# Kernel tuning notes

Hardware: AMD Instinct MI355X
Metric: run time of the kernel (lower is better)

The kernel has to match this reference:

```python
import jax, jax.numpy as jnp
import numpy as np

V, D, DC, L, K, H, ND, S, B = 16, 256, 128, 3, 16, 4, 3, 900, 16
HD = D // H
DMETA = 17           # [confidence(1) | layer_id(8) | iter(4) | pass(4)]
DSLOT = DC + DMETA
MAX_ITERS, MAX_PASSES, WRITE_TOK = 2, 2, 64
FLOATS = ['token_embed','segment_embed','slot_embeddings','layer_id_embeddings',
          'Wq_read','Wk_read','Wv_read','Wg_read','bg_read','Wqkv','Wo',
          'Wwk','Wwv','Wwg','bwg','Wout','bout','prev_answer_embed','Wfb','bfb']


def setup_inputs():
    key = jax.random.key(0)
    ks = jax.random.split(key, 24)
    n = lambda i, shape: 0.02 * jax.random.normal(ks[i], shape, dtype=jnp.float32)
    return dict(
        demo_inputs=jax.random.randint(ks[0], (B, ND, S), 0, V),
        demo_outputs=jax.random.randint(ks[1], (B, ND, S), 0, V),
        test_input=jax.random.randint(ks[2], (B, S), 0, V),
        token_embed=n(3, (V, D)), segment_embed=n(4, (2, D)),
        slot_embeddings=n(5, (L, K, DC)), layer_id_embeddings=n(6, (L, 8)),
        Wq_read=n(7, (L, D, DC)), Wk_read=n(8, (L, DSLOT, DC)), Wv_read=n(9, (L, DSLOT, D)),
        Wg_read=n(10, (L, D, 1)), bg_read=jnp.zeros((L, 1)),
        Wqkv=n(11, (L, D, 3 * D)), Wo=n(12, (L, D, D)),
        Wwk=n(13, (L, D, DC)), Wwv=n(14, (L, D, DC)),
        Wwg=n(15, (L, 2 * DC, 1)), bwg=jnp.zeros((L, 1)),
        Wout=n(16, (D, V)), bout=jnp.zeros((V,)),
        prev_answer_embed=n(17, (V, D)),
        Wfb=n(18, (2 * D, D)), bfb=jnp.zeros((D,)),
    )


def make_rope(n, hd):
    inv = 1.0 / (10000.0 ** (jnp.arange(0, hd, 2, dtype=jnp.float32) / hd))
    f = jnp.arange(n, dtype=jnp.float32)[:, None] * inv[None, :]  # [N, hd/2]
    return jnp.cos(f), jnp.sin(f)


def apply_rope(x, cos, sin):  # x: [B,H,N,hd]
    x1, x2 = x[..., ::2], x[..., 1::2]
    r1 = x1 * cos - x2 * sin
    r2 = x1 * sin + x2 * cos
    return jnp.stack([r1, r2], axis=-1).reshape(x.shape)


def layer_step(h, cache, l, it, pas, cos, sin, p):
    Bsz, N, _ = h.shape
    s0 = l * K
    # --- read: cross-attention from sequence to full structured cache ---
    q = h @ p['Wq_read'][l]                                   # [B,N,DC]
    k = cache @ p['Wk_read'][l]                               # [B,LK,DC]
    v = cache @ p['Wv_read'][l]                               # [B,LK,D]
    attn = jax.nn.softmax(jnp.einsum('bnd,bmd->bnm', q, k) / np.float32(np.sqrt(DC)), axis=-1)
    read = jnp.einsum('bnm,bmd->bnd', attn, v)
    rgate = jax.nn.sigmoid(h @ p['Wg_read'][l] + p['bg_read'][l])
    h = h + rgate * read
    # --- linear self-attention with RoPE (use_linear_attention=True) ---
    qh, kh, vh = jnp.split(h @ p['Wqkv'][l], 3, axis=-1)
    heads = lambda x: x.reshape(Bsz, N, H, HD).transpose(0, 2, 1, 3)
    qh, kh, vh = heads(qh), heads(kh), heads(vh)
    qf = jax.nn.elu(apply_rope(qh, cos, sin)) + 1.0
    kf = jax.nn.elu(apply_rope(kh, cos, sin)) + 1.0
    kv = jnp.einsum('bhnd,bhne->bhde', kf, vh)                # [B,H,HD,HD]
    z = 1.0 / (jnp.einsum('bhnd,bhd->bhn', qf, kf.sum(axis=2)) + 1e-6)
    att = jnp.einsum('bhnd,bhde->bhne', qf, kv) * z[..., None]
    h = h + att.transpose(0, 2, 1, 3).reshape(Bsz, N, D) @ p['Wo'][l]
    # --- write: last max_write_tokens tokens -> this layer's slot block ---
    wt = h[:, -WRITE_TOK:]                                    # [B,64,D]
    wk, wv = wt @ p['Wwk'][l], wt @ p['Wwv'][l]               # [B,64,DC]
    sq = cache[:, s0:s0 + K, :DC]                             # slot content queries
    wattn = jax.nn.softmax(jnp.einsum('bkd,bmd->bkm', sq, wk) / np.float32(np.sqrt(DC)), axis=-1)
    new_c = jnp.einsum('bkm,bmd->bkd', wattn, wv)
    wgate = jax.nn.sigmoid(jnp.concatenate([sq, new_c], -1) @ p['Wwg'][l] + p['bwg'][l])
    it_oh = jax.nn.one_hot(min(it, 3), 4, dtype=h.dtype)
    ps_oh = jax.nn.one_hot(min(pas, 3), 4, dtype=h.dtype)
    cache = cache.at[:, s0:s0 + K, :DC].set(sq + wgate * new_c)
    cache = cache.at[:, s0:s0 + K, DC:DC + 1].set(wgate)      # confidence
    cache = cache.at[:, s0:s0 + K, DC + 9:DC + 13].set(jnp.broadcast_to(it_oh, (Bsz, K, 4)))
    cache = cache.at[:, s0:s0 + K, DC + 13:].set(jnp.broadcast_to(ps_oh, (Bsz, K, 4)))
    return h, cache


def _model(p, demo_inputs, demo_outputs, test_input):
    Bsz = test_input.shape[0]
    # interleave demo_in/demo_out pairs then append test input
    demos = jnp.stack([demo_inputs, demo_outputs], axis=2).reshape(Bsz, ND * 2 * S)
    full = jnp.concatenate([demos, test_input], axis=1)       # [B, 6300]
    N = full.shape[1]
    cur = p['token_embed'][full] + p['segment_embed'][0]      # [B,N,D]
    cos, sin = make_rope(N, HD)
    # initial cache: learned content | conf=0 | layer_id | iter=0 | pass=0
    content = jnp.broadcast_to(p['slot_embeddings'].reshape(L * K, DC), (Bsz, L * K, DC))
    lids = jnp.broadcast_to(p['layer_id_embeddings'][:, None, :], (L, K, 8)).reshape(L * K, 8)
    meta = jnp.concatenate([jnp.zeros((L * K, 1)), lids, jnp.zeros((L * K, 8))], axis=-1)
    cache = jnp.concatenate([content, jnp.broadcast_to(meta, (Bsz, L * K, DMETA))], axis=-1)
    ts = ND * 2 * S
    prev_logits = None
    for pas in range(MAX_PASSES):
        if pas > 0:  # answer feedback from previous pass predictions
            pae = p['prev_answer_embed'][jnp.argmax(prev_logits, axis=-1)]
            tr = cur[:, ts:ts + S]
            g = jax.nn.sigmoid(jnp.concatenate([tr, pae], -1) @ p['Wfb'] + p['bfb'])
            cur = cur.at[:, ts:ts + S].set(tr + g * pae)
        h = cur
        for l in range(L):
            for it in range(MAX_ITERS):
                h, cache = layer_step(h, cache, l, it, pas, cos, sin, p)
        prev_logits = h[:, ts:ts + S] @ p['Wout'] + p['bout']  # [B,S,V]
    return prev_logits


def reference(demo_inputs, demo_outputs, test_input, token_embed, segment_embed,
              slot_embeddings, layer_id_embeddings, Wq_read, Wk_read, Wv_read,
              Wg_read, bg_read, Wqkv, Wo, Wwk, Wwv, Wwg, bwg, Wout, bout,
              prev_answer_embed, Wfb, bfb):
    p = dict(zip(FLOATS, (token_embed, segment_embed, slot_embeddings, layer_id_embeddings,
                          Wq_read, Wk_read, Wv_read, Wg_read, bg_read, Wqkv, Wo,
                          Wwk, Wwv, Wwg, bwg, Wout, bout, prev_answer_embed, Wfb, bfb)))
    return _model(p, demo_inputs, demo_outputs, test_input)
```

## Files before the change

kernel.cpp:

```cpp
#include <hip/hip_runtime.h>
#include <math.h>

#define Bz 16
#define Sz 900
#define Vz 16
#define Dz 256
#define DCz 128
#define Hz 4
#define Nz 6300
#define TSz 5400
#define DSLOTz 145
#define NSLOTz 48
#define GXA 99

typedef unsigned short u16;
typedef unsigned int u32;

typedef __bf16 bf16x8 __attribute__((ext_vector_type(8)));
typedef float floatx4 __attribute__((ext_vector_type(4)));
union U8 { bf16x8 v; uint4 q; };

static __device__ __forceinline__ float sigm(float x){ return 1.0f/(1.0f+__expf(-x)); }
static __device__ __forceinline__ void fma4(float4& a, float s, float4 b){ a.x+=s*b.x; a.y+=s*b.y; a.z+=s*b.z; a.w+=s*b.w; }
static __device__ __forceinline__ float dot4(float4 a, float4 b){ return a.x*b.x + a.y*b.y + a.z*b.z + a.w*b.w; }
static __device__ __forceinline__ float4 f4z(){ float4 z; z.x=0.f; z.y=0.f; z.z=0.f; z.w=0.f; return z; }
static __device__ __forceinline__ float elu1(float x){ return x>0.f ? x+1.f : __expf(x); }
static __device__ __forceinline__ float fcomp(float4 v, int i){ return (i==0)?v.x:(i==1)?v.y:(i==2)?v.z:v.w; }

static __device__ __forceinline__ uint hi16(float x){
  uint u = __float_as_uint(x);
  return (u + 0x7fffu + ((u>>16)&1u)) >> 16;
}

typedef const void GV __attribute__((address_space(1)));
typedef void LV __attribute__((address_space(3)));
static __device__ __forceinline__ void gl16(const float* g, float* l){
  __builtin_amdgcn_global_load_lds((GV*)g, (LV*)l, 16, 0, 0);
}
static __device__ __forceinline__ void gl16b(const void* g, void* l){
  __builtin_amdgcn_global_load_lds((GV*)g, (LV*)l, 16, 0, 0);
}

__global__ void k_sentinel(float* out, int nelem){
  int i = blockIdx.x*256 + threadIdx.x;
  if (i < nelem) out[i] = 12345.0f;
}

__global__ void k_zero(float* p, int n){
  int i = blockIdx.x*256 + threadIdx.x;
  if (i < n) p[i] = 0.f;
}

__global__ void k_rope(float* cost, float* sint){
  int i = blockIdx.x*256 + threadIdx.x;
  if (i >= Nz*32) return;
  int n = i>>5, f = i&31;
  double invd = pow(10000.0, -(double)f/32.0);
  double fr = (double)n * invd;
  cost[i] = (float)cos(fr);
  sint[i] = (float)sin(fr);
}

__global__ void k_embed(const int* __restrict__ di, const int* __restrict__ dq,
                        const int* __restrict__ ti, const float* __restrict__ temb,
                        const float* __restrict__ semb, float* __restrict__ h){
  int i = blockIdx.x*256 + threadIdx.x;
  if (i >= Bz*Nz*64) return;
  int dv = i & 63; int bn = i >> 6; int n = bn % Nz; int b = bn / Nz;
  int tok;
  if (n < TSz){
    int nd = n/1800; int r = n - nd*1800;
    tok = (r < Sz) ? di[(b*3+nd)*Sz + r] : dq[(b*3+nd)*Sz + (r-Sz)];
  } else {
    tok = ti[b*Sz + (n-TSz)];
  }
  const float4* e4 = (const float4*)(temb + (size_t)tok*Dz);
  const float4* s4 = (const float4*)semb;
  float4 v = e4[dv]; float4 s = s4[dv];
  v.x += s.x; v.y += s.y; v.z += s.z; v.w += s.w;
  ((float4*)h)[(size_t)bn*64 + dv] = v;
}

__global__ void k_cache_init(const float* __restrict__ slot_emb, const float* __restrict__ lid,
                             float* __restrict__ cache){
  int i = blockIdx.x*256 + threadIdx.x;
  if (i >= Bz*NSLOTz*DSLOTz) return;
  int c = i % DSLOTz; int sc = (i / DSLOTz) % NSLOTz; int l = sc >> 4;
  float v = 0.f;
  if (c < DCz) v = slot_emb[sc*DCz + c];
  else if (c >= 129 && c < 137) v = lid[l*8 + (c-129)];
  cache[i] = v;
}

__global__ void k_pack_w(const float* __restrict__ Wqkv,
                         u16* __restrict__ wh, u16* __restrict__ wl){
  int i = blockIdx.x*256 + threadIdx.x;
  if (i >= 3*65536) return;
  int l = i >> 16; int r = i & 65535;
  int ks = r >> 13; int ct = (r>>9)&15; int lane = (r>>3)&63; int e = r&7;
  int k = ks*32 + ((lane>>4)<<3) + e;
  int c = ct*16 + (lane&15);
  float x = Wqkv[(size_t)l*196608 + (size_t)k*768 + c];
  uint hb = hi16(x);
  uint lb = hi16(x - __uint_as_float(hb<<16));
  wh[i] = (u16)hb; wl[i] = (u16)lb;
}

__global__ void k_pack_wkv(const float* __restrict__ Wqkv,
                           u16* __restrict__ wh, u16* __restrict__ wl){
  int i = blockIdx.x*256 + threadIdx.x;
  if (i >= 3*131072) return;
  int l = i / 131072; int r = i % 131072;
  int ks = r >> 14; int ct = (r>>9)&31; int lane = (r>>3)&63; int e = r&7;
  int k = ks*32 + ((lane>>4)<<3) + e;
  int c = ct*16 + (lane&15);
  float x = Wqkv[(size_t)l*196608 + (size_t)k*768 + 256 + c];
  uint hb = hi16(x);
  uint lb = hi16(x - __uint_as_float(hb<<16));
  wh[i] = (u16)hb; wl[i] = (u16)lb;
}

__global__ void k_pack_wr(const float* __restrict__ Wqr,
                          u16* __restrict__ wh, u16* __restrict__ wl){
  int i = blockIdx.x*256 + threadIdx.x;
  if (i >= 3*32768) return;
  int l = i >> 15; int r = i & 32767;
  int ks = r >> 12; int ct = (r>>9)&7; int lane = (r>>3)&63; int e = r&7;
  int k = ks*32 + ((lane>>4)<<3) + e;
  int c = ct*16 + (lane&15);
  float x = Wqr[(size_t)l*32768 + (size_t)k*DCz + c];
  uint hb = hi16(x);
  uint lb = hi16(x - __uint_as_float(hb<<16));
  wh[i] = (u16)hb; wl[i] = (u16)lb;
}

__global__ void k_pack_p(const float* __restrict__ pmat,
                         u16* __restrict__ ph, u16* __restrict__ pl){
  int i = blockIdx.x*256 + threadIdx.x;
  if (i >= 16*65536) return;
  int b = i >> 16; int r = i & 65535;
  int ks2 = r >> 13; int ct = (r>>9)&15; int lane = (r>>3)&63; int e = r&7;
  int c = ks2*32 + ((lane>>4)<<3) + e;
  int oc = ct*16 + (lane&15);
  float x = pmat[(((size_t)(b*4 + (c>>6)))*64 + (c&63))*256 + oc];
  uint hb = hi16(x);
  uint lb = hi16(x - __uint_as_float(hb<<16));
  ph[i] = (u16)hb; pl[i] = (u16)lb;
}

__global__ __launch_bounds__(384) void k_proj_cache(const float* __restrict__ cache,
    const float* __restrict__ Wk, const float* __restrict__ Wv,
    u16* __restrict__ krh, u16* __restrict__ krl,
    u16* __restrict__ vrh, u16* __restrict__ vrl){
  __shared__ float crow[DSLOTz];
  int b = blockIdx.x / NSLOTz, sc = blockIdx.x % NSLOTz;
  int t = threadIdx.x;
  const float* cp = cache + (size_t)(b*NSLOTz+sc)*DSLOTz;
  if (t < DSLOTz) crow[t] = cp[t];
  __syncthreads();
  if (t < DCz){
    float a = 0.f;
    for (int r2=0;r2<DSLOTz;r2++) a += crow[r2]*Wk[r2*DCz + t];
    uint hb = hi16(a);
    uint lb = hi16(a - __uint_as_float(hb<<16));
    int ks = t>>5, st = sc>>4, lane = (sc&15) | (((t>>3)&3)<<4), e = t&7;
    size_t idx = (size_t)b*6144 + (size_t)(((ks*3+st)*64 + lane)*8 + e);
    krh[idx] = (u16)hb; krl[idx] = (u16)lb;
  } else {
    int d = t - DCz;
    float a = 0.f;
    for (int r2=0;r2<DSLOTz;r2++) a += crow[r2]*Wv[r2*Dz + d];
    uint hb = hi16(a);
    uint lb = hi16(a - __uint_as_float(hb<<16));
    int ot = d>>4, ks2 = sc>>5, lane = (d&15) | (((sc>>3)&3)<<4), e = sc&7;
    size_t idx = (size_t)b*16384 + (size_t)(((ks2*16+ot)*64 + lane)*8 + e);
    vrh[idx] = (u16)hb; vrl[idx] = (u16)lb;
  }
}

#define RA2_BH 0
#define RA2_BL 5120
#define RA2_QBH 10240
#define RA2_QBL 30720
#define RA2_ABH 10240
#define RA2_ABL 20480
#define RA2_G  51200
#define RA2_WG 51456
__global__ __launch_bounds__(256) void k_read_attn(
    float* __restrict__ h,
    const u16* __restrict__ wqh, const u16* __restrict__ wql,
    const u16* __restrict__ krh, const u16* __restrict__ krl,
    const u16* __restrict__ vrh, const u16* __restrict__ vrl,
    const float* __restrict__ Wg, const float* __restrict__ bg,
    float* __restrict__ kvbuf){
  __shared__ float smem[13120];
  char* sb = (char*)smem;
  const int t = threadIdx.x;
  const int b = blockIdx.y;
  const int n0 = blockIdx.x*64;
  const int w = t>>6, lane = t&63, ln = t&15, lq = (t>>4)&3;
  float* hb = h + (size_t)b*Nz*Dz;
  {
    int gid = (b*GXA + blockIdx.x)*256 + t;
    if (gid < Bz*Hz*4160) kvbuf[gid] = 0.f;
  }
  ((float*)(sb+RA2_WG))[t] = Wg[t];
  floatx4 acc[2][4];
  #pragma unroll
  for (int i=0;i<2;i++)
    #pragma unroll
    for (int j=0;j<4;j++){ acc[i][j][0]=0.f; acc[i][j][1]=0.f; acc[i][j][2]=0.f; acc[i][j][3]=0.f; }
  for (int ks=0; ks<8; ks++){
    __syncthreads();
    {
      int n = n0 + (t>>2);
      const float* hp = hb + (size_t)n*Dz + ks*32 + (t&3)*8;
      float x[8];
      if (n < Nz){
        float4 v0 = *(const float4*)(hp);
        float4 v1 = *(const float4*)(hp+4);
        x[0]=v0.x; x[1]=v0.y; x[2]=v0.z; x[3]=v0.w;
        x[4]=v1.x; x[5]=v1.y; x[6]=v1.z; x[7]=v1.w;
      } else {
        #pragma unroll
        for (int e=0;e<8;e++) x[e]=0.f;
      }
      uint hw[4], lw[4];
      #pragma unroll
      for (int e=0;e<4;e++){
        uint h0=hi16(x[2*e]), h1=hi16(x[2*e+1]);
        uint l0=hi16(x[2*e]-__uint_as_float(h0<<16));
        uint l1=hi16(x[2*e+1]-__uint_as_float(h1<<16));
        hw[e]=h0|(h1<<16); lw[e]=l0|(l1<<16);
      }
      int a16 = (((t>>2)*5 + (t&3))<<4);
      *(uint4*)(sb + RA2_BH + a16) = make_uint4(hw[0],hw[1],hw[2],hw[3]);
      *(uint4*)(sb + RA2_BL + a16) = make_uint4(lw[0],lw[1],lw[2],lw[3]);
    }
    __syncthreads();
    U8 bh[4], bl[4];
    #pragma unroll
    for (int nt=0; nt<4; nt++){
      int a16 = (((nt*16+ln)*5 + lq)<<4);
      bh[nt].q = *(const uint4*)(sb + RA2_BH + a16);
      bl[nt].q = *(const uint4*)(sb + RA2_BL + a16);
    }
    #pragma unroll
    for (int mf=0; mf<2; mf++){
      U8 ah, al;
      size_t ai = ((size_t)(ks*8 + w*2 + mf))*512 + lane*8;
      ah.q = *(const uint4*)(wqh + ai);
      al.q = *(const uint4*)(wql + ai);
      #pragma unroll
      for (int nt=0; nt<4; nt++){
        acc[mf][nt] = __builtin_amdgcn_mfma_f32_16x16x32_bf16(ah.v, bh[nt].v, acc[mf][nt], 0,0,0);
        acc[mf][nt] = __builtin_amdgcn_mfma_f32_16x16x32_bf16(ah.v, bl[nt].v, acc[mf][nt], 0,0,0);
        acc[mf][nt] = __builtin_amdgcn_mfma_f32_16x16x32_bf16(al.v, bh[nt].v, acc[mf][nt], 0,0,0);
      }
    }
  }
  {
    int n = t>>2, kq = t&3;
    int nn = n0+n; int nc = (nn < Nz) ? nn : (Nz-1);
    const float* hp = hb + (size_t)nc*Dz + kq*64;
    const float* wgp = (const float*)(sb+RA2_WG) + kq*64;
    float a = 0.f;
    for (int k=0;k<64;k+=4){
      float4 hv = *(const float4*)(hp+k);
      float4 wv = *(const float4*)(wgp+k);
      a += dot4(hv,wv);
    }
    a += __shfl_xor(a,1,64);
    a += __shfl_xor(a,2,64);
    if (kq==0) ((float*)(sb+RA2_G))[n] = a;
  }
  {
    #pragma unroll
    for (int mf=0; mf<2; mf++){
      #pragma unroll
      for (int nt=0; nt<4; nt++){
        float v0 = acc[mf][nt][0], v1 = acc[mf][nt][1];
        float v2 = acc[mf][nt][2], v3 = acc[mf][nt][3];
        uint h0=hi16(v0), h1=hi16(v1), h2=hi16(v2), h3=hi16(v3);
        uint l0=hi16(v0-__uint_as_float(h0<<16));
        uint l1=hi16(v1-__uint_as_float(h1<<16));
        uint l2=hi16(v2-__uint_as_float(h2<<16));
        uint l3=hi16(v3-__uint_as_float(h3<<16));
        int a16 = (((nt*16+ln)*5 + (mf*2 + (lq>>1)))<<4) + ((lq&1)<<3);
        *(uint2*)(sb + RA2_QBH + w*5120 + a16) = make_uint2(h0|(h1<<16), h2|(h3<<16));
        *(uint2*)(sb + RA2_QBL + w*5120 + a16) = make_uint2(l0|(l1<<16), l2|(l3<<16));
      }
    }
  }
  __syncthreads();
  floatx4 sacc[3];
  #pragma unroll
  for (int st=0; st<3; st++){ sacc[st][0]=0.f; sacc[st][1]=0.f; sacc[st][2]=0.f; sacc[st][3]=0.f; }
  for (int ks=0; ks<4; ks++){
    U8 bh, bl;
    int a16 = (((w*16+ln)*5 + lq)<<4);
    bh.q = *(const uint4*)(sb + RA2_QBH + ks*5120 + a16);
    bl.q = *(const uint4*)(sb + RA2_QBL + ks*5120 + a16);
    #pragma unroll
    for (int st=0; st<3; st++){
      U8 ah, al;
      size_t ai = (size_t)b*6144 + ((size_t)(ks*3+st))*512 + lane*8;
      ah.q = *(const uint4*)(krh + ai);
      al.q = *(const uint4*)(krl + ai);
      sacc[st] = __builtin_amdgcn_mfma_f32_16x16x32_bf16(ah.v, bh.v, sacc[st], 0,0,0);
      sacc[st] = __builtin_amdgcn_mfma_f32_16x16x32_bf16(ah.v, bl.v, sacc[st], 0,0,0);
      sacc[st] = __builtin_amdgcn_mfma_f32_16x16x32_bf16(al.v, bh.v, sacc[st], 0,0,0);
    }
  }
  {
    const float scl = 0.088388347648318447f;
    float mx = -1e30f;
    #pragma unroll
    for (int st=0; st<3; st++)
      #pragma unroll
      for (int r=0;r<4;r++){ sacc[st][r] *= scl; mx = fmaxf(mx, sacc[st][r]); }
    mx = fmaxf(mx, __shfl_xor(mx, 16, 64));
    mx = fmaxf(mx, __shfl_xor(mx, 32, 64));
    float su = 0.f;
    #pragma unroll
    for (int st=0; st<3; st++)
      #pragma unroll
      for (int r=0;r<4;r++){ float e = __expf(sacc[st][r]-mx); sacc[st][r]=e; su+=e; }
    su += __shfl_xor(su, 16, 64);
    su += __shfl_xor(su, 32, 64);
    float inv = 1.f/su;
    #pragma unroll
    for (int st=0; st<3; st++)
      #pragma unroll
      for (int r=0;r<4;r++) sacc[st][r] *= inv;
  }
  __syncthreads();
  {
    uint2 ah2[3], al2[3];
    #pragma unroll
    for (int st=0; st<3; st++){
      float v0=sacc[st][0], v1=sacc[st][1], v2=sacc[st][2], v3=sacc[st][3];
      uint h0=hi16(v0), h1=hi16(v1), h2=hi16(v2), h3=hi16(v3);
      uint l0=hi16(v0-__uint_as_float(h0<<16));
      uint l1=hi16(v1-__uint_as_float(h1<<16));
      uint l2=hi16(v2-__uint_as_float(h2<<16));
      uint l3=hi16(v3-__uint_as_float(h3<<16));
      ah2[st] = make_uint2(h0|(h1<<16), h2|(h3<<16));
      al2[st] = make_uint2(l0|(l1<<16), l2|(l3<<16));
    }
    int rb = (w*16+ln)*5;
    int sub = (lq&1)<<3;
    #pragma unroll
    for (int st=0; st<2; st++){
      int a16 = ((rb + st*2 + (lq>>1))<<4) + sub;
      *(uint2*)(sb + RA2_ABH + a16) = ah2[st];
      *(uint2*)(sb + RA2_ABL + a16) = al2[st];
    }
    {
      int a16 = ((rb + (lq>>1))<<4) + sub;
      *(uint2*)(sb + RA2_ABH + 5120 + a16) = ah2[2];
      *(uint2*)(sb + RA2_ABL + 5120 + a16) = al2[2];
      int z16 = ((rb + 2 + (lq>>1))<<4) + sub;
      *(uint2*)(sb + RA2_ABH + 5120 + z16) = make_uint2(0,0);
      *(uint2*)(sb + RA2_ABL + 5120 + z16) = make_uint2(0,0);
    }
  }
  __syncthreads();
  floatx4 o[4][4];
  #pragma unroll
  for (int i=0;i<4;i++)
    #pragma unroll
    for (int j=0;j<4;j++){ o[i][j][0]=0.f; o[i][j][1]=0.f; o[i][j][2]=0.f; o[i][j][3]=0.f; }
  #pragma unroll
  for (int ks2=0; ks2<2; ks2++){
    U8 bh[4], bl[4];
    #pragma unroll
    for (int nt=0; nt<4; nt++){
      int a16 = (((nt*16+ln)*5 + lq)<<4);
      bh[nt].q = *(const uint4*)(sb + RA2_ABH + ks2*5120 + a16);
      bl[nt].q = *(const uint4*)(sb + RA2_ABL + ks2*5120 + a16);
    }
    #pragma unroll
    for (int mf=0; mf<4; mf++){
      U8 ah, al;
      size_t ai = (size_t)b*16384 + ((size_t)(ks2*16 + w*4 + mf))*512 + lane*8;
      ah.q = *(const uint4*)(vrh + ai);
      al.q = *(const uint4*)(vrl + ai);
      #pragma unroll
      for (int nt=0; nt<4; nt++){
        o[mf][nt] = __builtin_amdgcn_mfma_f32_16x16x32_bf16(ah.v, bh[nt].v, o[mf][nt], 0,0,0);
        o[mf][nt] = __builtin_amdgcn_mfma_f32_16x16x32_bf16(ah.v, bl[nt].v, o[mf][nt], 0,0,0);
        o[mf][nt] = __builtin_amdgcn_mfma_f32_16x16x32_bf16(al.v, bh[nt].v, o[mf][nt], 0,0,0);
      }
    }
  }
  float bg0 = bg[0];
  #pragma unroll
  for (int nt=0; nt<4; nt++){
    int n = n0 + nt*16 + ln;
    if (n < Nz){
      float gv = sigm(((const float*)(sb+RA2_G))[nt*16+ln] + bg0);
      #pragma unroll
      for (int mf=0; mf<4; mf++){
        float* hp = hb + (size_t)n*Dz + w*64 + mf*16 + lq*4;
        float4 hv = *(const float4*)hp;
        hv.x += gv*o[mf][nt][0];
        hv.y += gv*o[mf][nt][1];
        hv.z += gv*o[mf][nt][2];
        hv.w += gv*o[mf][nt][3];
        *(float4*)hp = hv;
      }
    }
  }
}

__global__ __launch_bounds__(256) void k_kv(
    const float* __restrict__ h,
    const u16* __restrict__ wh, const u16* __restrict__ wl,
    const float* __restrict__ cost, const float* __restrict__ sint,
    float* __restrict__ kvbuf){
  __shared__ float smem[8704];
  char* sb = (char*)smem;
  const int t = threadIdx.x;
  const int b = blockIdx.y;
  const int n0 = blockIdx.x*64;
  const int w = t>>6;
  const int lane = t&63;
  const int ln = t&15;
  const int lq = (t>>4)&3;
  const float* hb = h + (size_t)b*Nz*Dz;
  floatx4 acc[2][4][4];
  #pragma unroll
  for (int cp=0;cp<2;cp++)
    #pragma unroll
    for (int i=0;i<4;i++)
      #pragma unroll
      for (int j=0;j<4;j++){ acc[cp][i][j][0]=0.f; acc[cp][i][j][1]=0.f; acc[cp][i][j][2]=0.f; acc[cp][i][j][3]=0.f; }

  const int hrow = t>>2, hcol = t&3;
  const float* hbase = hb + (size_t)(n0+hrow)*Dz + hcol*8;
  const int hvalid = (n0+hrow) < Nz;
  const int a16w = ((hrow*5 + hcol)<<4);

  auto load_h = [&](int ks, float x[8]){
    if (hvalid){
      float4 v0 = *(const float4*)(hbase + ks*32);
      float4 v1 = *(const float4*)(hbase + ks*32 + 4);
      x[0]=v0.x; x[1]=v0.y; x[2]=v0.z; x[3]=v0.w;
      x[4]=v1.x; x[5]=v1.y; x[6]=v1.z; x[7]=v1.w;
    } else {
      #pragma unroll
      for (int e=0;e<8;e++) x[e]=0.f;
    }
  };
  auto cvt_write = [&](const float x[8], int buf){
    uint hw[4], lw[4];
    #pragma unroll
    for (int e=0;e<4;e++){
      uint h0=hi16(x[2*e]), h1=hi16(x[2*e+1]);
      uint l0=hi16(x[2*e]-__uint_as_float(h0<<16));
      uint l1=hi16(x[2*e+1]-__uint_as_float(h1<<16));
      hw[e]=h0|(h1<<16); lw[e]=l0|(l1<<16);
    }
    *(uint4*)(sb + buf*10240 + a16w) = make_uint4(hw[0],hw[1],hw[2],hw[3]);
    *(uint4*)(sb + buf*10240 + 5120 + a16w) = make_uint4(lw[0],lw[1],lw[2],lw[3]);
  };

  { float x0[8]; load_h(0, x0); cvt_write(x0, 0); }
  for (int ks=0; ks<8; ks++){
    __syncthreads();
    float xn[8];
    if (ks < 7) load_h(ks+1, xn);
    const int cb = ks&1;
    U8 bh[4], bl[4];
    #pragma unroll
    for (int nt=0; nt<4; nt++){
      int a16 = (((nt*16+ln)*5 + lq)<<4);
      bh[nt].q = *(const uint4*)(sb + cb*10240 + a16);
      bl[nt].q = *(const uint4*)(sb + cb*10240 + 5120 + a16);
    }
    #pragma unroll
    for (int cp=0; cp<2; cp++){
      #pragma unroll
      for (int mf=0; mf<4; mf++){
        U8 ah, al;
        size_t ai = ((size_t)(ks*32 + cp*16 + w*4 + mf))*512 + lane*8;
        ah.q = *(const uint4*)(wh + ai);
        al.q = *(const uint4*)(wl + ai);
        #pragma unroll
        for (int nt=0; nt<4; nt++){
          acc[cp][mf][nt] = __builtin_amdgcn_mfma_f32_16x16x32_bf16(ah.v, bh[nt].v, acc[cp][mf][nt], 0,0,0);
          acc[cp][mf][nt] = __builtin_amdgcn_mfma_f32_16x16x32_bf16(ah.v, bl[nt].v, acc[cp][mf][nt], 0,0,0);
          acc[cp][mf][nt] = __builtin_amdgcn_mfma_f32_16x16x32_bf16(al.v, bh[nt].v, acc[cp][mf][nt], 0,0,0);
        }
      }
    }
    if (ks < 7) cvt_write(xn, cb^1);
  }
  #pragma unroll
  for (int mf=0; mf<4; mf++){
    #pragma unroll
    for (int nt=0; nt<4; nt++){
      int n = n0 + nt*16 + ln;
      int valid = (n < Nz);
      int nc = valid ? n : (Nz-1);
      int pi = mf*8 + lq*2;
      float2 c2 = *(const float2*)(cost + (size_t)nc*32 + pi);
      float2 s2 = *(const float2*)(sint + (size_t)nc*32 + pi);
      float q0 = acc[0][mf][nt][0], q1 = acc[0][mf][nt][1];
      float q2 = acc[0][mf][nt][2], q3 = acc[0][mf][nt][3];
      float r0 = elu1(q0*c2.x - q1*s2.x);
      float r1 = elu1(q0*s2.x + q1*c2.x);
      float r2 = elu1(q2*c2.y - q3*s2.y);
      float r3 = elu1(q2*s2.y + q3*c2.y);
      acc[0][mf][nt][0] = valid ? r0 : 0.f;
      acc[0][mf][nt][1] = valid ? r1 : 0.f;
      acc[0][mf][nt][2] = valid ? r2 : 0.f;
      acc[0][mf][nt][3] = valid ? r3 : 0.f;
    }
  }
  const int d = t&63, q4 = t>>6;
  float* kfL = smem;
  float* vL  = smem + 4352;
  for (int g=0; g<4; g++){
    __syncthreads();
    if (w == g){
      #pragma unroll
      for (int mf=0; mf<4; mf++){
        #pragma unroll
        for (int nt=0; nt<4; nt++){
          int n = nt*16 + ln;
          int cc = mf*16 + lq*4;
          *(float4*)(kfL + n*68 + cc) = make_float4(acc[0][mf][nt][0],acc[0][mf][nt][1],acc[0][mf][nt][2],acc[0][mf][nt][3]);
          *(float4*)(vL  + n*68 + cc) = make_float4(acc[1][mf][nt][0],acc[1][mf][nt][1],acc[1][mf][nt][2],acc[1][mf][nt][3]);
        }
      }
    }
    __syncthreads();
    float4 kvacc[4];
    #pragma unroll
    for (int u=0;u<4;u++) kvacc[u]=f4z();
    float ksl = 0.f;
    for (int row=0; row<64; row++){
      float kd = kfL[row*68 + d];
      ksl += kd;
      const float4* vp = (const float4*)(vL + row*68);
      #pragma unroll
      for (int u=0;u<4;u++) fma4(kvacc[u], kd, vp[q4*4+u]);
    }
    float* kq = kvbuf + ((size_t)(b*Hz + g))*4160;
    #pragma unroll
    for (int u=0;u<4;u++){
      int e = q4*16 + 4*u;
      atomicAdd(&kq[(e+0)*64+d], kvacc[u].x);
      atomicAdd(&kq[(e+1)*64+d], kvacc[u].y);
      atomicAdd(&kq[(e+2)*64+d], kvacc[u].z);
      atomicAdd(&kq[(e+3)*64+d], kvacc[u].w);
    }
    if (q4==0) atomicAdd(&kq[4096+d], ksl);
  }
}

__global__ __launch_bounds__(256) void k_pmat(const float* __restrict__ kvbuf,
    const float* __restrict__ Wo, float* __restrict__ pmat){
  __shared__ float smem[8448];
  const int t = threadIdx.x;
  const int bh = blockIdx.x;
  const int hh = bh & 3;
  const int c0 = t&15, rr = t>>4;
  const float* kvp = kvbuf + (size_t)bh*4160;
  for (int id=t; id<4096; id+=256){
    int e=id>>6, d=id&63;
    smem[e*68+d] = kvp[id];
  }
  float4 acc[4][4];
  #pragma unroll
  for (int i=0;i<4;i++){
    #pragma unroll
    for (int j=0;j<4;j++) acc[i][j]=f4z();
  }
  for (int kt=0; kt<64; kt+=16){
    __syncthreads();
    for (int id=t; id<1024; id+=256){
      int wr=id>>6, cf=id&63;
      ((float4*)(smem+4352))[wr*64+cf] = ((const float4*)(Wo + (size_t)(hh*64+kt+wr)*256))[cf];
    }
    __syncthreads();
    for (int kk=0; kk<16; kk++){
      float4 a4 = *(const float4*)(smem + (kt+kk)*68 + 4*rr);
      const float4* wrow = (const float4*)(smem+4352) + kk*64;
      float4 w0=wrow[c0], w1=wrow[c0+16], w2=wrow[c0+32], w3=wrow[c0+48];
      #pragma unroll
      for (int i=0;i<4;i++){
        float ac = fcomp(a4,i);
        fma4(acc[i][0],ac,w0); fma4(acc[i][1],ac,w1); fma4(acc[i][2],ac,w2); fma4(acc[i][3],ac,w3);
      }
    }
  }
  float* Pp = pmat + (size_t)bh*16384;
  #pragma unroll
  for (int i=0;i<4;i++){
    #pragma unroll
    for (int j=0;j<4;j++) ((float4*)Pp)[(4*rr+i)*64 + c0 + 16*j] = acc[i][j];
  }
}

#define AH_OFF 0
#define AL_OFF 16384
#define BH_OFF 32768
#define BL_OFF 37888
#define KS_OFF 43008
__global__ __launch_bounds__(256) void k_att(
    float* __restrict__ h,
    const u16* __restrict__ wqh, const u16* __restrict__ wql,
    const u16* __restrict__ pth, const u16* __restrict__ ptl,
    const float* __restrict__ kvbuf,
    const float* __restrict__ cost, const float* __restrict__ sint){
  __shared__ float smem[11008];
  char* sb = (char*)smem;
  const int t = threadIdx.x;
  const int b = blockIdx.y;
  const int n0 = blockIdx.x*64;
  const int w = t>>6;
  const int lane = t&63;
  const int ln = t&15;
  const int lq = (t>>4)&3;
  float* hb = h + (size_t)b*Nz*Dz;
  ((float*)(sb+KS_OFF))[t] = kvbuf[(size_t)(b*Hz + w)*4160 + 4096 + lane];
  floatx4 acc[4][4];
  #pragma unroll
  for (int i=0;i<4;i++)
    #pragma unroll
    for (int j=0;j<4;j++){ acc[i][j][0]=0.f; acc[i][j][1]=0.f; acc[i][j][2]=0.f; acc[i][j][3]=0.f; }

  for (int ks=0; ks<8; ks++){
    __syncthreads();
    const u16* sh = wqh + (size_t)ks*8192;
    const u16* sl = wql + (size_t)ks*8192;
    #pragma unroll
    for (int j=0;j<4;j++){
      int c = w*4 + j;
      gl16b(sh + c*512 + lane*8, sb + AH_OFF + c*1024);
      gl16b(sl + c*512 + lane*8, sb + AL_OFF + c*1024);
    }
    {
      int n = n0 + (t>>2);
      const float* hp = hb + (size_t)n*Dz + ks*32 + (t&3)*8;
      float x[8];
      if (n < Nz){
        float4 v0 = *(const float4*)(hp);
        float4 v1 = *(const float4*)(hp+4);
        x[0]=v0.x; x[1]=v0.y; x[2]=v0.z; x[3]=v0.w;
        x[4]=v1.x; x[5]=v1.y; x[6]=v1.z; x[7]=v1.w;
      } else {
        #pragma unroll
        for (int e=0;e<8;e++) x[e]=0.f;
      }
      uint hw[4], lw[4];
      #pragma unroll
      for (int e=0;e<4;e++){
        uint h0=hi16(x[2*e]), h1=hi16(x[2*e+1]);
        uint l0=hi16(x[2*e]-__uint_as_float(h0<<16));
        uint l1=hi16(x[2*e+1]-__uint_as_float(h1<<16));
        hw[e]=h0|(h1<<16); lw[e]=l0|(l1<<16);
      }
      int a16 = (((t>>2)*5 + (t&3))<<4);
      *(uint4*)(sb + BH_OFF + a16) = make_uint4(hw[0],hw[1],hw[2],hw[3]);
      *(uint4*)(sb + BL_OFF + a16) = make_uint4(lw[0],lw[1],lw[2],lw[3]);
    }
    __syncthreads();
    U8 bh[4], bl[4];
    #pragma unroll
    for (int nt=0; nt<4; nt++){
      int a16 = (((nt*16+ln)*5 + lq)<<4);
      bh[nt].q = *(const uint4*)(sb + BH_OFF + a16);
      bl[nt].q = *(const uint4*)(sb + BL_OFF + a16);
    }
    #pragma unroll
    for (int mf=0; mf<4; mf++){
      U8 ah, al;
      int a16 = (((w*4+mf)*64 + lane)<<4);
      ah.q = *(const uint4*)(sb + AH_OFF + a16);
      al.q = *(const uint4*)(sb + AL_OFF + a16);
      #pragma unroll
      for (int nt=0; nt<4; nt++){
        acc[mf][nt] = __builtin_amdgcn_mfma_f32_16x16x32_bf16(ah.v, bh[nt].v, acc[mf][nt], 0,0,0);
        acc[mf][nt] = __builtin_amdgcn_mfma_f32_16x16x32_bf16(ah.v, bl[nt].v, acc[mf][nt], 0,0,0);
        acc[mf][nt] = __builtin_amdgcn_mfma_f32_16x16x32_bf16(al.v, bh[nt].v, acc[mf][nt], 0,0,0);
      }
    }
  }
  uint2 qzh[4][4], qzl[4][4];
  {
    float4 ks4[4];
    #pragma unroll
    for (int mf=0; mf<4; mf++)
      ks4[mf] = *(const float4*)(sb + KS_OFF + ((w*64 + mf*16 + lq*4)<<2));
    float psum[4] = {0.f,0.f,0.f,0.f};
    #pragma unroll
    for (int mf=0; mf<4; mf++){
      #pragma unroll
      for (int nt=0; nt<4; nt++){
        int n = n0 + nt*16 + ln;
        int nc = (n < Nz) ? n : (Nz-1);
        int pi = mf*8 + lq*2;
        float2 c2 = *(const float2*)(cost + (size_t)nc*32 + pi);
        float2 s2 = *(const float2*)(sint + (size_t)nc*32 + pi);
        float q0 = acc[mf][nt][0], q1 = acc[mf][nt][1];
        float q2 = acc[mf][nt][2], q3 = acc[mf][nt][3];
        float r0 = elu1(q0*c2.x - q1*s2.x);
        float r1 = elu1(q0*s2.x + q1*c2.x);
        float r2 = elu1(q2*c2.y - q3*s2.y);
        float r3 = elu1(q2*s2.y + q3*c2.y);
        acc[mf][nt][0]=r0; acc[mf][nt][1]=r1; acc[mf][nt][2]=r2; acc[mf][nt][3]=r3;
        psum[nt] += r0*ks4[mf].x + r1*ks4[mf].y + r2*ks4[mf].z + r3*ks4[mf].w;
      }
    }
    float zt[4];
    #pragma unroll
    for (int nt=0; nt<4; nt++){
      float p = psum[nt];
      p += __shfl_xor(p, 16, 64);
      p += __shfl_xor(p, 32, 64);
      zt[nt] = 1.f/(p + 1e-6f);
    }
    #pragma unroll
    for (int mf=0; mf<4; mf++){
      #pragma unroll
      for (int nt=0; nt<4; nt++){
        float v0 = acc[mf][nt][0]*zt[nt];
        float v1 = acc[mf][nt][1]*zt[nt];
        float v2 = acc[mf][nt][2]*zt[nt];
        float v3 = acc[mf][nt][3]*zt[nt];
        uint h0=hi16(v0), h1=hi16(v1), h2=hi16(v2), h3=hi16(v3);
        qzh[mf][nt] = make_uint2(h0|(h1<<16), h2|(h3<<16));
        uint l0=hi16(v0-__uint_as_float(h0<<16));
        uint l1=hi16(v1-__uint_as_float(h1<<16));
        uint l2=hi16(v2-__uint_as_float(h2<<16));
        uint l3=hi16(v3-__uint_as_float(h3<<16));
        qzl[mf][nt] = make_uint2(l0|(l1<<16), l2|(l3<<16));
      }
    }
  }
  floatx4 acc2[4][4];
  #pragma unroll
  for (int i=0;i<4;i++)
    #pragma unroll
    for (int j=0;j<4;j++){ acc2[i][j][0]=0.f; acc2[i][j][1]=0.f; acc2[i][j][2]=0.f; acc2[i][j][3]=0.f; }
  for (int ks2=0; ks2<8; ks2++){
    __syncthreads();
    const u16* sh = pth + (size_t)(b*8 + ks2)*8192;
    const u16* sl = ptl + (size_t)(b*8 + ks2)*8192;
    #pragma unroll
    for (int j=0;j<4;j++){
      int c = w*4 + j;
      gl16b(sh + c*512 + lane*8, sb + AH_OFF + c*1024);
      gl16b(sl + c*512 + lane*8, sb + AL_OFF + c*1024);
    }
    if (w == (ks2>>1)){
      #pragma unroll
      for (int mm=0; mm<2; mm++){
        int mf = ((ks2&1)<<1) + mm;
        int g = (mm<<1) + (lq>>1);
        int sub = (lq&1)*8;
        #pragma unroll
        for (int nt=0; nt<4; nt++){
          int a16 = (((nt*16+ln)*5 + g)<<4) + sub;
          *(uint2*)(sb + BH_OFF + a16) = qzh[mf][nt];
          *(uint2*)(sb + BL_OFF + a16) = qzl[mf][nt];
        }
      }
    }
    __syncthreads();
    U8 bh[4], bl[4];
    #pragma unroll
    for (int nt=0; nt<4; nt++){
      int a16 = (((nt*16+ln)*5 + lq)<<4);
      bh[nt].q = *(const uint4*)(sb + BH_OFF + a16);
      bl[nt].q = *(const uint4*)(sb + BL_OFF + a16);
    }
    #pragma unroll
    for (int mf=0; mf<4; mf++){
      U8 ah, al;
      int a16 = (((w*4+mf)*64 + lane)<<4);
      ah.q = *(const uint4*)(sb + AH_OFF + a16);
      al.q = *(const uint4*)(sb + AL_OFF + a16);
      #pragma unroll
      for (int nt=0; nt<4; nt++){
        acc2[mf][nt] = __builtin_amdgcn_mfma_f32_16x16x32_bf16(ah.v, bh[nt].v, acc2[mf][nt], 0,0,0);
        acc2[mf][nt] = __builtin_amdgcn_mfma_f32_16x16x32_bf16(ah.v, bl[nt].v, acc2[mf][nt], 0,0,0);
        acc2[mf][nt] = __builtin_amdgcn_mfma_f32_16x16x32_bf16(al.v, bh[nt].v, acc2[mf][nt], 0,0,0);
      }
    }
  }
  #pragma unroll
  for (int mf=0; mf<4; mf++){
    #pragma unroll
    for (int nt=0; nt<4; nt++){
      int n = n0 + nt*16 + ln;
      if (n < Nz){
        float* hp = hb + (size_t)n*Dz + w*64 + mf*16 + lq*4;
        float4 hv = *(const float4*)hp;
        hv.x += acc2[mf][nt][0];
        hv.y += acc2[mf][nt][1];
        hv.z += acc2[mf][nt][2];
        hv.w += acc2[mf][nt][3];
        *(float4*)hp = hv;
      }
    }
  }
}

__global__ __launch_bounds__(256) void k_wkv(const float* __restrict__ h,
    const float* __restrict__ Wwk, const float* __restrict__ Wwv,
    float* __restrict__ wkbuf, float* __restrict__ wvbuf){
  __shared__ float wtL[16*257];
  int t = threadIdx.x;
  int b = blockIdx.y, m0 = blockIdx.x*16;
  const float* hb = h + ((size_t)b*Nz + (Nz-64))*Dz;
  for (int i=t;i<16*Dz;i+=256){ int r=i>>8,c=i&255; wtL[r*257+c] = hb[(size_t)(m0+r)*Dz + c]; }
  __syncthreads();
  int r=t>>4, c0=t&15;
  float4 ak0=f4z(),ak1=f4z(),av0=f4z(),av1=f4z();
  for (int kk=0;kk<Dz;kk++){
    float hv = wtL[r*257+kk];
    const float4* wk4 = (const float4*)(Wwk + (size_t)kk*DCz);
    const float4* wv4 = (const float4*)(Wwv + (size_t)kk*DCz);
    fma4(ak0,hv,wk4[c0]); fma4(ak1,hv,wk4[c0+16]);
    fma4(av0,hv,wv4[c0]); fma4(av1,hv,wv4[c0+16]);
  }
  float4* ok = (float4*)(wkbuf + (size_t)(b*64 + m0+r)*DCz);
  float4* ov = (float4*)(wvbuf + (size_t)(b*64 + m0+r)*DCz);
  ok[c0]=ak0; ok[c0+16]=ak1; ov[c0]=av0; ov[c0+16]=av1;
}

__global__ __launch_bounds__(256) void k_cache_upd(float* __restrict__ cache,
    const float* __restrict__ wkbuf, const float* __restrict__ wvbuf,
    const float* __restrict__ Wwg, const float* __restrict__ bwg,
    int s0, int it, int pas){
  __shared__ float sqL[16*132];
  __shared__ float wkL[64*132];
  __shared__ float wat[16*68];
  __shared__ float ncL[16*132];
  __shared__ float wg[16];
  int t = threadIdx.x; int b = blockIdx.x;
  for (int i=t;i<16*DCz;i+=256){ int k2=i>>7,c=i&127; sqL[k2*132+c] = cache[((size_t)(b*NSLOTz)+s0+k2)*DSLOTz + c]; }
  for (int i=t;i<64*DCz;i+=256){ int m=i>>7,c=i&127; wkL[m*132+c] = wkbuf[(size_t)(b*64+m)*DCz+c]; }
  __syncthreads();
  {
    int k2 = t>>4;
    const float4* s4 = (const float4*)(sqL) + k2*33;
    for (int mm=0;mm<4;mm++){
      int m = (t&15) + 16*mm;
      const float4* k4 = (const float4*)(wkL) + m*33;
      float a=0.f;
      for (int d4=0;d4<32;d4++) a += dot4(s4[d4], k4[d4]);
      wat[k2*68+m] = a * 0.088388347648318447f;
    }
  }
  __syncthreads();
  if (t<16){
    float mx=-1e30f;
    for (int m=0;m<64;m++) mx = fmaxf(mx, wat[t*68+m]);
    float su=0.f;
    for (int m=0;m<64;m++){ float e=__expf(wat[t*68+m]-mx); wat[t*68+m]=e; su+=e; }
    float inv=1.f/su;
    for (int m=0;m<64;m++) wat[t*68+m]*=inv;
  }
  __syncthreads();
  {
    int k2=t>>4, c0=t&15;
    float4 a0=f4z(), a1=f4z();
    const float4* wvg = (const float4*)(wvbuf + (size_t)b*64*DCz);
    for (int m=0;m<64;m++){
      float a = wat[k2*68+m];
      fma4(a0,a,wvg[m*32+c0]); fma4(a1,a,wvg[m*32+c0+16]);
    }
    ((float4*)ncL)[k2*33+c0]=a0; ((float4*)ncL)[k2*33+16+c0]=a1;
  }
  __syncthreads();
  if (t<16){
    float a = bwg[0];
    for (int d2=0; d2<DCz; d2++) a += sqL[t*132+d2]*Wwg[d2] + ncL[t*132+d2]*Wwg[DCz+d2];
    wg[t] = sigm(a);
  }
  __syncthreads();
  for (int i=t;i<16*DCz;i+=256){
    int k2=i>>7,c=i&127;
    cache[((size_t)(b*NSLOTz)+s0+k2)*DSLOTz + c] = sqL[k2*132+c] + wg[k2]*ncL[k2*132+c];
  }
  if (t<16){
    float* cp = cache + ((size_t)(b*NSLOTz)+s0+t)*DSLOTz;
    cp[128] = wg[t];
    cp[137] = (it==0)?1.f:0.f; cp[138] = (it==1)?1.f:0.f; cp[139]=0.f; cp[140]=0.f;
    cp[141] = (pas==0)?1.f:0.f; cp[142] = (pas==1)?1.f:0.f; cp[143]=0.f; cp[144]=0.f;
  }
}

__global__ __launch_bounds__(256) void k_logits(const float* __restrict__ h,
    const float* __restrict__ Wout, const float* __restrict__ bout, float* __restrict__ out){
  __shared__ float hl[16*257];
  int t = threadIdx.x; int row0 = blockIdx.x*16;
  for (int i=t;i<16*Dz;i+=256){
    int rr=i>>8,c=i&255; int row=row0+rr; int b=row/Sz, s=row-b*Sz;
    hl[rr*257+c] = h[((size_t)b*Nz + TSz + s)*Dz + c];
  }
  __syncthreads();
  int rr = t>>4, v = t&15;
  float a = bout[v];
  for (int c=0;c<Dz;c++) a += hl[rr*257+c]*Wout[c*Vz + v];
  out[(size_t)(row0+rr)*Vz + v] = a;
}

__global__ __launch_bounds__(256) void k_feedback(float* __restrict__ h,
    const float* __restrict__ logits0, const float* __restrict__ pae,
    const float* __restrict__ Wfb, const float* __restrict__ bfb){
  __shared__ float trL[16*257];
  __shared__ float paeL[16*257];
  __shared__ int amL[16];
  int t = threadIdx.x; int b = blockIdx.y; int s0 = blockIdx.x*16;
  if (t<16){
    int s = s0+t; int am=0;
    if (s < Sz){
      const float* lg = logits0 + (size_t)(b*Sz+s)*Vz;
      float best = lg[0];
      for (int v=1;v<16;v++){ if (lg[v] > best){ best=lg[v]; am=v; } }
    }
    amL[t]=am;
  }
  for (int i=t;i<16*Dz;i+=256){
    int rr=i>>8,c=i&255; int s=s0+rr;
    trL[rr*257+c] = (s<Sz)? h[((size_t)b*Nz + TSz + s)*Dz + c] : 0.f;
  }
  __syncthreads();
  for (int i=t;i<16*Dz;i+=256){ int rr=i>>8,c=i&255; paeL[rr*257+c] = pae[(size_t)amL[rr]*Dz + c]; }
  __syncthreads();
  int r=t>>4, c0=t&15;
  float4 acc[4]; acc[0]=f4z(); acc[1]=f4z(); acc[2]=f4z(); acc[3]=f4z();
  for (int kk=0;kk<Dz;kk++){
    float xv = trL[r*257+kk];
    const float4* wr = (const float4*)(Wfb + (size_t)kk*Dz);
    fma4(acc[0],xv,wr[c0]); fma4(acc[1],xv,wr[c0+16]); fma4(acc[2],xv,wr[c0+32]); fma4(acc[3],xv,wr[c0+48]);
  }
  for (int kk=0;kk<Dz;kk++){
    float xv = paeL[r*257+kk];
    const float4* wr = (const float4*)(Wfb + (size_t)(Dz+kk)*Dz);
    fma4(acc[0],xv,wr[c0]); fma4(acc[1],xv,wr[c0+16]); fma4(acc[2],xv,wr[c0+32]); fma4(acc[3],xv,wr[c0+48]);
  }
  int s = s0+r;
  if (s < Sz){
    float* cp = h + ((size_t)b*Nz + TSz + s)*Dz;
    #pragma unroll
    for (int j=0;j<4;j++){
      float vals[4] = {acc[j].x, acc[j].y, acc[j].z, acc[j].w};
      #pragma unroll
      for (int q2=0;q2<4;q2++){
        int c = (c0+16*j)*4 + q2;
        float g = sigm(vals[q2] + bfb[c]);
        cp[c] = trL[r*257+c] + g*paeL[r*257+c];
      }
    }
  }
}

extern "C" void kernel_launch(void* const* d_in, const int* in_sizes, int n_in,
                              void* d_out, int out_size, void* d_ws, size_t ws_size,
                              hipStream_t stream){
  (void)in_sizes; (void)n_in;
  const int*   demo_in   = (const int*)d_in[0];
  const int*   demo_out  = (const int*)d_in[1];
  const int*   test_in   = (const int*)d_in[2];
  const float* token_emb = (const float*)d_in[3];
  const float* seg_emb   = (const float*)d_in[4];
  const float* slot_emb  = (const float*)d_in[5];
  const float* lid_emb   = (const float*)d_in[6];
  const float* Wq_read   = (const float*)d_in[7];
  const float* Wk_read   = (const float*)d_in[8];
  const float* Wv_read   = (const float*)d_in[9];
  const float* Wg_read   = (const float*)d_in[10];
  const float* bg_read   = (const float*)d_in[11];
  const float* Wqkv      = (const float*)d_in[12];
  const float* Wo        = (const float*)d_in[13];
  const float* Wwk       = (const float*)d_in[14];
  const float* Wwv       = (const float*)d_in[15];
  const float* Wwg       = (const float*)d_in[16];
  const float* bwg       = (const float*)d_in[17];
  const float* Wout      = (const float*)d_in[18];
  const float* bout      = (const float*)d_in[19];
  const float* pae       = (const float*)d_in[20];
  const float* Wfb       = (const float*)d_in[21];
  const float* bfb       = (const float*)d_in[22];

  char* wsb = (char*)d_ws;
  size_t off = 0;
  auto alloc = [&](size_t bytes)->char*{
    char* p = wsb + off;
    off += (bytes + 255) & ~(size_t)255;
    return p;
  };
  float* hbuf   = (float*)alloc((size_t)Bz*Nz*Dz*4);
  float* cache  = (float*)alloc((size_t)Bz*NSLOTz*DSLOTz*4);
  float* kvbuf  = (float*)alloc((size_t)Bz*Hz*4160*4);
  float* pmat   = (float*)alloc((size_t)Bz*Hz*64*256*4);
  float* wkbuf  = (float*)alloc((size_t)Bz*64*DCz*4);
  float* wvbuf  = (float*)alloc((size_t)Bz*64*DCz*4);
  float* logits0= (float*)alloc((size_t)Bz*Sz*Vz*4);
  float* cost   = (float*)alloc((size_t)Nz*32*4);
  float* sint   = (float*)alloc((size_t)Nz*32*4);
  u16*   wqth   = (u16*)alloc((size_t)3*65536*2);
  u16*   wqtl   = (u16*)alloc((size_t)3*65536*2);
  u16*   pth    = (u16*)alloc((size_t)16*65536*2);
  u16*   ptl    = (u16*)alloc((size_t)16*65536*2);
  u16*   wkvh   = (u16*)alloc((size_t)3*131072*2);
  u16*   wkvl   = (u16*)alloc((size_t)3*131072*2);
  u16*   wqrh   = (u16*)alloc((size_t)3*32768*2);
  u16*   wqrl   = (u16*)alloc((size_t)3*32768*2);
  u16*   krh    = (u16*)alloc((size_t)Bz*6144*2);
  u16*   krl    = (u16*)alloc((size_t)Bz*6144*2);
  u16*   vrh    = (u16*)alloc((size_t)Bz*16384*2);
  u16*   vrl    = (u16*)alloc((size_t)Bz*16384*2);

  if (off > ws_size){
    k_sentinel<<<(out_size+255)/256, 256, 0, stream>>>((float*)d_out, out_size);
    return;
  }

  k_rope<<<(Nz*32+255)/256, 256, 0, stream>>>(cost, sint);
  k_cache_init<<<(Bz*NSLOTz*DSLOTz+255)/256, 256, 0, stream>>>(slot_emb, lid_emb, cache);
  k_pack_w<<<768, 256, 0, stream>>>(Wqkv, wqth, wqtl);
  k_pack_wkv<<<1536, 256, 0, stream>>>(Wqkv, wkvh, wkvl);
  k_pack_wr<<<384, 256, 0, stream>>>(Wq_read, wqrh, wqrl);
  k_zero<<<512, 256, 0, stream>>>((float*)vrh, Bz*16384/2);
  k_zero<<<512, 256, 0, stream>>>((float*)vrl, Bz*16384/2);

  for (int pas=0; pas<2; pas++){
    k_embed<<<(Bz*Nz*64+255)/256, 256, 0, stream>>>(demo_in, demo_out, test_in, token_emb, seg_emb, hbuf);
    if (pas==1)
      k_feedback<<<dim3(57,Bz), 256, 0, stream>>>(hbuf, logits0, pae, Wfb, bfb);
    for (int l=0; l<3; l++){
      for (int it=0; it<2; it++){
        k_proj_cache<<<Bz*NSLOTz, 384, 0, stream>>>(cache,
            Wk_read + (size_t)l*DSLOTz*DCz, Wv_read + (size_t)l*DSLOTz*Dz,
            krh, krl, vrh, vrl);
        k_read_attn<<<dim3(GXA,Bz), 256, 0, stream>>>(hbuf,
            wqrh + (size_t)l*32768, wqrl + (size_t)l*32768,
            krh, krl, vrh, vrl,
            Wg_read + (size_t)l*Dz, bg_read + l, kvbuf);
        k_kv<<<dim3(GXA,Bz), 256, 0, stream>>>(hbuf,
            wkvh + (size_t)l*131072, wkvl + (size_t)l*131072, cost, sint, kvbuf);
        k_pmat<<<Bz*Hz, 256, 0, stream>>>(kvbuf, Wo + (size_t)l*Dz*Dz, pmat);
        k_pack_p<<<4096, 256, 0, stream>>>(pmat, pth, ptl);
        k_att<<<dim3(GXA,Bz), 256, 0, stream>>>(hbuf,
            wqth + (size_t)l*65536, wqtl + (size_t)l*65536, pth, ptl,
            kvbuf, cost, sint);
        k_wkv<<<dim3(4,Bz), 256, 0, stream>>>(hbuf,
            Wwk + (size_t)l*Dz*DCz, Wwv + (size_t)l*Dz*DCz, wkbuf, wvbuf);
        k_cache_upd<<<Bz, 256, 0, stream>>>(cache, wkbuf, wvbuf,
            Wwg + (size_t)l*2*DCz, bwg + l, l*16, it, pas);
      }
    }
    float* outp = (pas==0) ? logits0 : (float*)d_out;
    k_logits<<<900, 256, 0, stream>>>(hbuf, Wout, bout, outp);
  }
}
```

Measured before the change: 8.164 ms.

## Double-buffer B tiles in k_att and read A fragments directly from global

The attention kernel stops staging the weight A-fragments through LDS and has each wave load its MFMA A operands straight from global memory. The h-tile and qz B-operand staging is double-buffered, so the next slice is loaded and converted while the current slice is multiplied, which removes one barrier per k-step. LDS use falls from about 44KB to about 21KB, which may let more blocks fit per CU. The cost is global-load latency on the A operands inside the MFMA loop, with no LDS sharing of those loads across the block.

```diff
diff --git a/kernel.cpp b/kernel.cpp
--- a/kernel.cpp
+++ b/kernel.cpp
@@ -605,18 +605,14 @@
   }
 }
 
-#define AH_OFF 0
-#define AL_OFF 16384
-#define BH_OFF 32768
-#define BL_OFF 37888
-#define KS_OFF 43008
+#define KA_KS 20480
 __global__ __launch_bounds__(256) void k_att(
     float* __restrict__ h,
     const u16* __restrict__ wqh, const u16* __restrict__ wql,
     const u16* __restrict__ pth, const u16* __restrict__ ptl,
     const float* __restrict__ kvbuf,
     const float* __restrict__ cost, const float* __restrict__ sint){
-  __shared__ float smem[11008];
+  __shared__ float smem[5376];
   char* sb = (char*)smem;
   const int t = threadIdx.x;
   const int b = blockIdx.y;
@@ -626,62 +622,61 @@
   const int ln = t&15;
   const int lq = (t>>4)&3;
   float* hb = h + (size_t)b*Nz*Dz;
-  ((float*)(sb+KS_OFF))[t] = kvbuf[(size_t)(b*Hz + w)*4160 + 4096 + lane];
+  ((float*)(sb+KA_KS))[t] = kvbuf[(size_t)(b*Hz + w)*4160 + 4096 + lane];
+
+  const int hrow = t>>2, hcol = t&3;
+  const float* hbase = hb + (size_t)(n0+hrow)*Dz + hcol*8;
+  const int hvalid = (n0+hrow) < Nz;
+  const int a16w = ((hrow*5 + hcol)<<4);
+  auto load_h = [&](int ks, float x[8]){
+    if (hvalid){
+      float4 v0 = *(const float4*)(hbase + ks*32);
+      float4 v1 = *(const float4*)(hbase + ks*32 + 4);
+      x[0]=v0.x; x[1]=v0.y; x[2]=v0.z; x[3]=v0.w;
+      x[4]=v1.x; x[5]=v1.y; x[6]=v1.z; x[7]=v1.w;
+    } else {
+      #pragma unroll
+      for (int e=0;e<8;e++) x[e]=0.f;
+    }
+  };
+  auto cvt_write = [&](const float x[8], int buf){
+    uint hw[4], lw[4];
+    #pragma unroll
+    for (int e=0;e<4;e++){
+      uint h0=hi16(x[2*e]), h1=hi16(x[2*e+1]);
+      uint l0=hi16(x[2*e]-__uint_as_float(h0<<16));
+      uint l1=hi16(x[2*e+1]-__uint_as_float(h1<<16));
+      hw[e]=h0|(h1<<16); lw[e]=l0|(l1<<16);
+    }
+    *(uint4*)(sb + buf*10240 + a16w) = make_uint4(hw[0],hw[1],hw[2],hw[3]);
+    *(uint4*)(sb + buf*10240 + 5120 + a16w) = make_uint4(lw[0],lw[1],lw[2],lw[3]);
+  };
+
   floatx4 acc[4][4];
   #pragma unroll
   for (int i=0;i<4;i++)
     #pragma unroll
     for (int j=0;j<4;j++){ acc[i][j][0]=0.f; acc[i][j][1]=0.f; acc[i][j][2]=0.f; acc[i][j][3]=0.f; }
 
+  { float x0[8]; load_h(0, x0); cvt_write(x0, 0); }
   for (int ks=0; ks<8; ks++){
     __syncthreads();
-    const u16* sh = wqh + (size_t)ks*8192;
-    const u16* sl = wql + (size_t)ks*8192;
-    #pragma unroll
-    for (int j=0;j<4;j++){
-      int c = w*4 + j;
-      gl16b(sh + c*512 + lane*8, sb + AH_OFF + c*1024);
-      gl16b(sl + c*512 + lane*8, sb + AL_OFF + c*1024);
-    }
-    {
-      int n = n0 + (t>>2);
-      const float* hp = hb + (size_t)n*Dz + ks*32 + (t&3)*8;
-      float x[8];
-      if (n < Nz){
-        float4 v0 = *(const float4*)(hp);
-        float4 v1 = *(const float4*)(hp+4);
-        x[0]=v0.x; x[1]=v0.y; x[2]=v0.z; x[3]=v0.w;
-        x[4]=v1.x; x[5]=v1.y; x[6]=v1.z; x[7]=v1.w;
-      } else {
-        #pragma unroll
-        for (int e=0;e<8;e++) x[e]=0.f;
-      }
-      uint hw[4], lw[4];
-      #pragma unroll
-      for (int e=0;e<4;e++){
-        uint h0=hi16(x[2*e]), h1=hi16(x[2*e+1]);
-        uint l0=hi16(x[2*e]-__uint_as_float(h0<<16));
-        uint l1=hi16(x[2*e+1]-__uint_as_float(h1<<16));
-        hw[e]=h0|(h1<<16); lw[e]=l0|(l1<<16);
-      }
-      int a16 = (((t>>2)*5 + (t&3))<<4);
-      *(uint4*)(sb + BH_OFF + a16) = make_uint4(hw[0],hw[1],hw[2],hw[3]);
-      *(uint4*)(sb + BL_OFF + a16) = make_uint4(lw[0],lw[1],lw[2],lw[3]);
-    }
-    __syncthreads();
+    float xn[8];
+    if (ks < 7) load_h(ks+1, xn);
+    const int cb = ks&1;
     U8 bh[4], bl[4];
     #pragma unroll
     for (int nt=0; nt<4; nt++){
       int a16 = (((nt*16+ln)*5 + lq)<<4);
-      bh[nt].q = *(const uint4*)(sb + BH_OFF + a16);
-      bl[nt].q = *(const uint4*)(sb + BL_OFF + a16);
+      bh[nt].q = *(const uint4*)(sb + cb*10240 + a16);
+      bl[nt].q = *(const uint4*)(sb + cb*10240 + 5120 + a16);
     }
     #pragma unroll
     for (int mf=0; mf<4; mf++){
       U8 ah, al;
-      int a16 = (((w*4+mf)*64 + lane)<<4);
-      ah.q = *(const uint4*)(sb + AH_OFF + a16);
-      al.q = *(const uint4*)(sb + AL_OFF + a16);
+      size_t ai = ((size_t)(ks*16 + w*4 + mf))*512 + lane*8;
+      ah.q = *(const uint4*)(wqh + ai);
+      al.q = *(const uint4*)(wql + ai);
       #pragma unroll
       for (int nt=0; nt<4; nt++){
         acc[mf][nt] = __builtin_amdgcn_mfma_f32_16x16x32_bf16(ah.v, bh[nt].v, acc[mf][nt], 0,0,0);
@@ -689,13 +684,14 @@
         acc[mf][nt] = __builtin_amdgcn_mfma_f32_16x16x32_bf16(al.v, bh[nt].v, acc[mf][nt], 0,0,0);
       }
     }
+    if (ks < 7) cvt_write(xn, cb^1);
   }
   uint2 qzh[4][4], qzl[4][4];
   {
     float4 ks4[4];
     #pragma unroll
     for (int mf=0; mf<4; mf++)
-      ks4[mf] = *(const float4*)(sb + KS_OFF + ((w*64 + mf*16 + lq*4)<<2));
+      ks4[mf] = *(const float4*)(sb + KA_KS + ((w*64 + mf*16 + lq*4)<<2));
     float psum[4] = {0.f,0.f,0.f,0.f};
     #pragma unroll
     for (int mf=0; mf<4; mf++){
@@ -742,49 +738,44 @@
       }
     }
   }
+  auto write_slice = [&](int s, int buf){
+    #pragma unroll
+    for (int mm=0; mm<2; mm++){
+      int mf = ((s&1)<<1) + mm;
+      int g = (mm<<1) + (lq>>1);
+      int sub = (lq&1)*8;
+      #pragma unroll
+      for (int nt=0; nt<4; nt++){
+        int a16 = (((nt*16+ln)*5 + g)<<4) + sub;
+        *(uint2*)(sb + buf*10240 + a16) = qzh[mf][nt];
+        *(uint2*)(sb + buf*10240 + 5120 + a16) = qzl[mf][nt];
+      }
+    }
+  };
   floatx4 acc2[4][4];
   #pragma unroll
   for (int i=0;i<4;i++)
     #pragma unroll
     for (int j=0;j<4;j++){ acc2[i][j][0]=0.f; acc2[i][j][1]=0.f; acc2[i][j][2]=0.f; acc2[i][j][3]=0.f; }
+  __syncthreads();
+  if (w == 0) write_slice(0, 0);
   for (int ks2=0; ks2<8; ks2++){
     __syncthreads();
-    const u16* sh = pth + (size_t)(b*8 + ks2)*8192;
-    const u16* sl = ptl + (size_t)(b*8 + ks2)*8192;
-    #pragma unroll
-    for (int j=0;j<4;j++){
-      int c = w*4 + j;
-      gl16b(sh + c*512 + lane*8, sb + AH_OFF + c*1024);
-      gl16b(sl + c*512 + lane*8, sb + AL_OFF + c*1024);
-    }
-    if (w == (ks2>>1)){
-      #pragma unroll
-      for (int mm=0; mm<2; mm++){
-        int mf = ((ks2&1)<<1) + mm;
-        int g = (mm<<1) + (lq>>1);
-        int sub = (lq&1)*8;
-        #pragma unroll
-        for (int nt=0; nt<4; nt++){
-          int a16 = (((nt*16+ln)*5 + g)<<4) + sub;
-          *(uint2*)(sb + BH_OFF + a16) = qzh[mf][nt];
-          *(uint2*)(sb + BL_OFF + a16) = qzl[mf][nt];
-        }
-      }
-    }
-    __syncthreads();
+    if (ks2 < 7 && w == ((ks2+1)>>1)) write_slice(ks2+1, (ks2+1)&1);
+    const int cb = ks2&1;
     U8 bh[4], bl[4];
     #pragma unroll
     for (int nt=0; nt<4; nt++){
       int a16 = (((nt*16+ln)*5 + lq)<<4);
-      bh[nt].q = *(const uint4*)(sb + BH_OFF + a16);
-      bl[nt].q = *(const uint4*)(sb + BL_OFF + a16);
+      bh[nt].q = *(const uint4*)(sb + cb*10240 + a16);
+      bl[nt].q = *(const uint4*)(sb + cb*10240 + 5120 + a16);
     }
     #pragma unroll
     for (int mf=0; mf<4; mf++){
       U8 ah, al;
-      int a16 = (((w*4+mf)*64 + lane)<<4);
-      ah.q = *(const uint4*)(sb + AH_OFF + a16);
-      al.q = *(const uint4*)(sb + AL_OFF + a16);
+      size_t ai = ((size_t)((b*8 + ks2)*16 + w*4 + mf))*512 + lane*8;
+      ah.q = *(const uint4*)(pth + ai);
+      al.q = *(const uint4*)(ptl + ai);
       #pragma unroll
       for (int nt=0; nt<4; nt++){
         acc2[mf][nt] = __builtin_amdgcn_mfma_f32_16x16x32_bf16(ah.v, bh[nt].v, acc2[mf][nt], 0,0,0);
```

Result: faster. 7.902 ms (-3.2%).
